# Kernel tuning notes

Measured on AMD Instinct MI355X. Metric: run time of the kernel, lower is better.

The kernel has to match this reference:

```python
import jax, jax.numpy as jnp
import numpy as np

EPS = 1e-5

def conv3x3(x, w, bias=None):
    y = jax.lax.conv_general_dilated(x, w, (1, 1), 'SAME',
                                     dimension_numbers=('NCHW', 'OIHW', 'NCHW'))
    if bias is not None:
        y = y + bias[None, :, None, None]
    return y

def batchnorm(x, g, b):
    m = x.mean((0, 2, 3), keepdims=True)
    v = x.var((0, 2, 3), keepdims=True)
    return (x - m) * jax.lax.rsqrt(v + EPS) * g[None, :, None, None] + b[None, :, None, None]

def deform_sample(x, offset, mask, dg=2):
    # x: [B,C,H,W]; offset: [B,dg*9*2,H,W] (dy,dx interleaved per mmcv); mask: [B,dg*9,H,W]
    B, C, H, W = x.shape
    K = 9
    cg = C // dg
    off = offset.reshape(B, dg, K, 2, H, W)
    dy, dx = off[:, :, :, 0], off[:, :, :, 1]
    m = mask.reshape(B, dg, K, H, W)
    ky = (jnp.repeat(jnp.arange(3), 3) - 1).astype(x.dtype)   # kernel row offset per tap
    kx = (jnp.tile(jnp.arange(3), 3) - 1).astype(x.dtype)     # kernel col offset per tap
    py = dy + jnp.arange(H, dtype=x.dtype)[None, None, None, :, None] + ky[None, None, :, None, None]
    px = dx + jnp.arange(W, dtype=x.dtype)[None, None, None, None, :] + kx[None, None, :, None, None]
    y0 = jnp.floor(py); x0 = jnp.floor(px)
    ly = py - y0; lx = px - x0
    y0i = y0.astype(jnp.int32); x0i = x0.astype(jnp.int32)
    y1i = y0i + 1; x1i = x0i + 1
    def ok(yy, xx):
        return ((yy >= 0) & (yy < H) & (xx >= 0) & (xx < W)).astype(x.dtype)
    xg = x.reshape(B, dg, cg, H * W)
    def gather(yy, xx):
        idx = (jnp.clip(yy, 0, H - 1) * W + jnp.clip(xx, 0, W - 1)).reshape(B, dg, -1)
        g = jax.vmap(jax.vmap(lambda im, ii: im[:, ii]))(xg, idx)   # [B,dg,cg,K*H*W]
        return g.reshape(B, dg, cg, K, H, W)
    w00 = ((1 - ly) * (1 - lx) * ok(y0i, x0i))[:, :, None]
    w01 = ((1 - ly) * lx * ok(y0i, x1i))[:, :, None]
    w10 = (ly * (1 - lx) * ok(y1i, x0i))[:, :, None]
    w11 = (ly * lx * ok(y1i, x1i))[:, :, None]
    val = (gather(y0i, x0i) * w00 + gather(y0i, x1i) * w01 +
           gather(y1i, x0i) * w10 + gather(y1i, x1i) * w11)
    return val * m[:, :, None]   # [B,dg,cg,K,H,W]

def reference(input_v, input_i, off_w, off_b, dconv_w, bn1_g, bn1_b, conv2_w, bn2_g, bn2_b):
    x = jnp.concatenate([input_v, input_i], axis=1)             # [B,C,H,W]
    off_all = conv3x3(x, off_w, off_b)                          # [B,54,H,W]
    o1, o2, mask = jnp.split(off_all, 3, axis=1)
    offset = jnp.concatenate([o1, o2], axis=1)                  # [B,36,H,W]
    mask = jax.nn.sigmoid(mask)                                 # [B,18,H,W]
    sampled = deform_sample(x, offset, mask, dg=2)              # [B,2,cg,9,H,W]
    O = dconv_w.shape[0]
    out = jnp.einsum('bgckhw,ogck->bohw', sampled, dconv_w.reshape(O, 2, -1, 9))
    out = jax.nn.relu(batchnorm(out, bn1_g, bn1_b))
    out = jax.nn.relu(batchnorm(conv3x3(out, conv2_w), bn2_g, bn2_b))
    return out

def setup_inputs() -> dict:
    key = jax.random.key(0)
    ks = jax.random.split(key, 8)
    B, Cm, O, H, W = 4, 128, 128, 64, 64
    C = 2 * Cm
    inp = {}
    inp['input_v'] = jax.random.normal(ks[0], (B, Cm, H, W), jnp.float32)
    inp['input_i'] = jax.random.normal(ks[1], (B, Cm, H, W), jnp.float32)
    # offset/mask conv (zero-init in torch; small random here for a non-trivial reference)
    inp['off_w'] = jax.random.normal(ks[2], (54, C, 3, 3), jnp.float32) * 0.02
    inp['off_b'] = jnp.zeros((54,), jnp.float32)
    inp['dconv_w'] = jax.random.normal(ks[3], (O, C, 3, 3), jnp.float32) * (1.0 / np.sqrt(C * 9))
    inp['bn1_g'] = jnp.ones((O,), jnp.float32)
    inp['bn1_b'] = jnp.zeros((O,), jnp.float32)
    inp['conv2_w'] = jax.random.normal(ks[4], (O, O, 3, 3), jnp.float32) * (1.0 / np.sqrt(O * 9))
    inp['bn2_g'] = jnp.ones((O,), jnp.float32)
    inp['bn2_b'] = jnp.zeros((O,), jnp.float32)
    return inp
```

## Files before the change

### kernel.cpp

```cpp
#include <hip/hip_runtime.h>

#define EPSBN 1e-5f

using s8v = __attribute__((ext_vector_type(8))) short;
using f4v = __attribute__((ext_vector_type(4))) float;

__device__ inline unsigned short f2bf(float f) {
  unsigned u = __float_as_uint(f);
  return (unsigned short)((u + 0x7FFFu + ((u >> 16) & 1u)) >> 16);
}

__global__ __launch_bounds__(256) void k_pack(const float* __restrict__ v, const float* __restrict__ im,
                                              unsigned short* __restrict__ xb) {
  __shared__ float tile[64][33];
  int b = blockIdx.z;
  int hw0 = blockIdx.x * 32;
  int c0 = blockIdx.y * 64;
  int tx = threadIdx.x, ty = threadIdx.y;
#pragma unroll
  for (int i = 0; i < 64; i += 8) {
    int c = c0 + ty + i;
    const float* src = (c < 128) ? (v + ((size_t)b * 128 + c) * 4096)
                                 : (im + ((size_t)b * 128 + (c - 128)) * 4096);
    tile[ty + i][tx] = src[hw0 + tx];
  }
  __syncthreads();
#pragma unroll
  for (int i = 0; i < 32; i += 8) {
    int hw = hw0 + ty + i;
    ushort2 o;
    o.x = f2bf(tile[2 * tx][ty + i]);
    o.y = f2bf(tile[2 * tx + 1][ty + i]);
    *(ushort2*)&xb[((size_t)(b * 4096 + hw)) * 256 + c0 + 2 * tx] = o;
  }
}

__global__ __launch_bounds__(256) void k_wprep_all(const float* __restrict__ w_off,
                                                   const float* __restrict__ w_d,
                                                   const float* __restrict__ w_2,
                                                   unsigned short* __restrict__ wt_off,
                                                   unsigned short* __restrict__ wt_d,
                                                   unsigned short* __restrict__ wt_2) {
  int bid = blockIdx.x, t = threadIdx.x;
  if (bid < 72) {
    int id = bid * 256 + t;
    int lane = id & 63;
    int nb = (id >> 6) & 3;
    int ks = id >> 8;
    int ks2 = ks & 1, tap = (ks >> 1) % 9, cc = ks / 18;
    int o = nb * 16 + (lane & 15);
    int cb = cc * 64 + ks2 * 32 + ((lane >> 4) * 8);
    s8v r;
#pragma unroll
    for (int j = 0; j < 8; ++j) {
      float val = (o < 54) ? w_off[((size_t)o * 256 + cb + j) * 9 + tap] : 0.f;
      r[j] = (short)f2bf(val);
    }
    *(s8v*)&wt_off[(size_t)id * 8] = r;
  } else if (bid < 216) {
    int id = (bid - 72) * 256 + t;
    int lane = id & 63;
    int nb = (id >> 6) & 7;
    int kstep = id >> 9;
    int chunk = kstep >> 2, ks4 = kstep & 3;
    int g = chunk / 9, kk = chunk % 9;
    int o = nb * 16 + (lane & 15);
    int cb = g * 128 + ks4 * 32 + ((lane >> 4) * 8);
    s8v r;
#pragma unroll
    for (int j = 0; j < 8; ++j) r[j] = (short)f2bf(w_d[((size_t)o * 256 + cb + j) * 9 + kk]);
    *(s8v*)&wt_d[(size_t)id * 8] = r;
  } else {
    int id = (bid - 216) * 256 + t;
    int lane = id & 63;
    int nb = (id >> 6) & 7;
    int kstep = id >> 9;
    int ks2 = kstep & 1, tap = (kstep >> 1) % 9, cc = kstep / 18;
    int o = nb * 16 + (lane & 15);
    int cb = cc * 64 + ks2 * 32 + ((lane >> 4) * 8);
    s8v r;
#pragma unroll
    for (int j = 0; j < 8; ++j) r[j] = (short)f2bf(w_2[((size_t)o * 128 + cb + j) * 9 + tap]);
    *(s8v*)&wt_2[(size_t)id * 8] = r;
  }
}

__global__ __launch_bounds__(512, 3) void k_offconv(const unsigned short* __restrict__ xb,
                                                    const unsigned short* __restrict__ wt,
                                                    const float* __restrict__ bias,
                                                    float* __restrict__ off) {
  __shared__ char Xs[102 * 512];
  __shared__ float redx[2048];
  int bid = blockIdx.x;
  int id8 = (bid & 7) * 64 + (bid >> 3);
  int w0 = (id8 & 1) * 32;
  int h = (id8 >> 1) & 63;
  int b = id8 >> 7;
  int t = threadIdx.x;
  int l = t & 63, wv = t >> 6;
  int og = wv & 3, kh = wv >> 2;
  f4v zero = {0.f, 0.f, 0.f, 0.f};
  f4v acc[2] = {zero, zero};

  for (int id = t; id < 3264; id += 512) {
    int tr = id >> 5, oq8 = id & 31;
    int ky = tr / 34, col = tr % 34;
    int hh = h + ky - 1, ww = w0 + col - 1;
    s8v val = {0, 0, 0, 0, 0, 0, 0, 0};
    if ((unsigned)hh < 64u && (unsigned)ww < 64u)
      val = *(const s8v*)&xb[(((size_t)(b * 64 + hh)) * 64 + ww) * 256 + oq8 * 8];
    int byte = (tr * 512 + oq8 * 16) ^ ((tr & 7) << 4);
    *(s8v*)(Xs + byte) = val;
  }
  __syncthreads();
  int khi = l >> 4, lo = l & 15;
#pragma unroll
  for (int tap = 0; tap < 9; ++tap) {
    int ky = tap / 3, kx = tap % 3;
#pragma unroll
    for (int s = 0; s < 4; ++s) {
      int cc = kh * 2 + (s >> 1);
      int ks2 = s & 1;
      int kstep = cc * 18 + tap * 2 + ks2;
      int chb = cc * 128 + ks2 * 64 + khi * 16;
      s8v bfr = *(const s8v*)&wt[((size_t)(kstep * 4 + og) * 64 + l) * 8];
#pragma unroll
      for (int m = 0; m < 2; ++m) {
        int tr = ky * 34 + m * 16 + lo + kx;
        int rbyte = (tr * 512 + chb) ^ ((tr & 7) << 4);
        s8v a = *(const s8v*)(Xs + rbyte);
        acc[m] = __builtin_amdgcn_mfma_f32_16x16x32_bf16(a, bfr, acc[m], 0, 0, 0);
      }
    }
  }
  if (kh == 1) {
#pragma unroll
    for (int m = 0; m < 2; ++m)
#pragma unroll
      for (int j = 0; j < 4; ++j) redx[((og * 64 + l) * 2 + m) * 4 + j] = acc[m][j];
  }
  __syncthreads();
  if (kh == 0) {
    int o = og * 16 + lo;
    int pixb = (b * 64 + h) * 64 + w0;
    if (o < 54) {
      float bi = bias[o];
#pragma unroll
      for (int m = 0; m < 2; ++m)
#pragma unroll
        for (int j = 0; j < 4; ++j) {
          int px = pixb + m * 16 + khi * 4 + j;
          float vv = acc[m][j] + redx[((og * 64 + l) * 2 + m) * 4 + j] + bi;
          if (o >= 36) vv = 1.f / (1.f + __expf(-vv));
          off[(size_t)px * 54 + o] = vv;
        }
    }
  }
}

#define DC_ISSUE(c, V, Q)                                   \
  do {                                                      \
    const unsigned* ip_ = sidx[(c)][px];                    \
    const float* qp_ = swt[(c)][px];                        \
    Q##0 = qp_[0]; Q##1 = qp_[1]; Q##2 = qp_[2]; Q##3 = qp_[3]; \
    V##0 = *(const s8v*)&xb[ip_[0] + chof];                 \
    V##1 = *(const s8v*)&xb[ip_[1] + chof];                 \
    V##2 = *(const s8v*)&xb[ip_[2] + chof];                 \
    V##3 = *(const s8v*)&xb[ip_[3] + chof];                 \
  } while (0)

#define DC_COMMIT(BUF, V, Q)                                            \
  do {                                                                  \
    unsigned rr_[4];                                                    \
    _Pragma("unroll") for (int jp_ = 0; jp_ < 4; ++jp_) {               \
      unsigned w0_ = ((const unsigned*)&V##0)[jp_];                     \
      unsigned w1_ = ((const unsigned*)&V##1)[jp_];                     \
      unsigned w2_ = ((const unsigned*)&V##2)[jp_];                     \
      unsigned w3_ = ((const unsigned*)&V##3)[jp_];                     \
      float e_ = Q##0 * __uint_as_float(w0_ << 16) + Q##1 * __uint_as_float(w1_ << 16) + \
                 Q##2 * __uint_as_float(w2_ << 16) + Q##3 * __uint_as_float(w3_ << 16);  \
      float o_ = Q##0 * __uint_as_float(w0_ & 0xffff0000u) + Q##1 * __uint_as_float(w1_ & 0xffff0000u) + \
                 Q##2 * __uint_as_float(w2_ & 0xffff0000u) + Q##3 * __uint_as_float(w3_ & 0xffff0000u);  \
      unsigned p_;                                                      \
      asm("v_cvt_pk_bf16_f32 %0, %1, %2" : "=v"(p_) : "v"(e_), "v"(o_)); \
      rr_[jp_] = p_;                                                    \
    }                                                                   \
    *(int4*)(&At[BUF][0] + wbyte) = *(int4*)rr_;                        \
  } while (0)

#define LDS_BARRIER()                                        \
  do {                                                       \
    asm volatile("s_waitcnt lgkmcnt(0)" ::: "memory");       \
    __builtin_amdgcn_s_barrier();                            \
  } while (0)

#define DC_MFMA(C, BUF)                                                 \
  do {                                                                  \
    __builtin_amdgcn_s_setprio(1);                                      \
    _Pragma("unroll") for (int ks4_ = 0; ks4_ < 4; ++ks4_) {            \
      int kstep_ = (C) * 4 + ks4_;                                      \
      s8v bfr_ = *(const s8v*)&wt[((size_t)(kstep_ * 8 + og) * 64 + l) * 8]; \
      int chb_ = ks4_ * 64 + khi * 16;                                  \
      _Pragma("unroll") for (int m_ = 0; m_ < 2; ++m_) {                \
        int trA_ = m_ * 16 + lo;                                        \
        int rbyte_ = (trA_ * 256 + chb_) ^ ((trA_ & 7) << 4);           \
        s8v a_ = *(const s8v*)(&At[BUF][0] + rbyte_);                   \
        acc[m_] = __builtin_amdgcn_mfma_f32_16x16x32_bf16(a_, bfr_, acc[m_], 0, 0, 0); \
      }                                                                 \
    }                                                                   \
    __builtin_amdgcn_s_setprio(0);                                      \
  } while (0)

#define DC_PHASE(C, BUF, VI, QI, VC, QC, BUFC)               \
  do {                                                       \
    if ((C) < 15) DC_ISSUE((C) + 3, VI, QI);                 \
    DC_MFMA(C, BUF);                                         \
    if ((C) < 17) DC_COMMIT(BUFC, VC, QC);                   \
    LDS_BARRIER();                                           \
  } while (0)

__global__ __launch_bounds__(512, 4) void k_dconv(const unsigned short* __restrict__ xb,
                                                  const float* __restrict__ off,
                                                  const unsigned short* __restrict__ wt,
                                                  float* __restrict__ y1p,
                                                  float* __restrict__ st1, float* __restrict__ st2) {
  __shared__ unsigned int sidx[18][32][4];
  __shared__ float swt[18][32][4];
  __shared__ char At[3][8192];
  int t = threadIdx.x;
  int l = t & 63, og = t >> 6;
  int bid = blockIdx.x;
  int id8 = (bid & 7) * 64 + (bid >> 3);
  int pixb = id8 * 32;
  int b = pixb >> 12, h = (pixb >> 6) & 63, w0 = pixb & 63;

  for (int id = t; id < 576; id += 512) {
    int chunk = id >> 5, ppx = id & 31;
    int g = chunk / 9, kk = chunk % 9;
    const float* op = off + (size_t)(pixb + ppx) * 54;
    float dy = op[(g * 9 + kk) * 2];
    float dx = op[(g * 9 + kk) * 2 + 1];
    float msk = op[36 + g * 9 + kk];
    float py = dy + (float)(h + kk / 3 - 1);
    float pxf = dx + (float)(w0 + ppx + kk % 3 - 1);
    float y0f = floorf(py), x0f = floorf(pxf);
    float ly = py - y0f, lx = pxf - x0f;
    int y0 = (int)y0f, x0 = (int)x0f;
    int y1 = y0 + 1, x1 = x0 + 1;
    float oky0 = (y0 >= 0 && y0 < 64) ? 1.f : 0.f;
    float oky1 = (y1 >= 0 && y1 < 64) ? 1.f : 0.f;
    float okx0 = (x0 >= 0 && x0 < 64) ? 1.f : 0.f;
    float okx1 = (x1 >= 0 && x1 < 64) ? 1.f : 0.f;
    int y0c = min(max(y0, 0), 63), y1c = min(max(y1, 0), 63);
    int x0c = min(max(x0, 0), 63), x1c = min(max(x1, 0), 63);
    unsigned base = (unsigned)(b * 4096);
    unsigned gofs = (unsigned)(g * 128);
    sidx[chunk][ppx][0] = (base + y0c * 64 + x0c) * 256u + gofs;
    sidx[chunk][ppx][1] = (base + y0c * 64 + x1c) * 256u + gofs;
    sidx[chunk][ppx][2] = (base + y1c * 64 + x0c) * 256u + gofs;
    sidx[chunk][ppx][3] = (base + y1c * 64 + x1c) * 256u + gofs;
    swt[chunk][ppx][0] = (1.f - ly) * (1.f - lx) * oky0 * okx0 * msk;
    swt[chunk][ppx][1] = (1.f - ly) * lx * oky0 * okx1 * msk;
    swt[chunk][ppx][2] = ly * (1.f - lx) * oky1 * okx0 * msk;
    swt[chunk][ppx][3] = ly * lx * oky1 * okx1 * msk;
  }
  __syncthreads();

  int px = t >> 4, oq = t & 15;
  unsigned chof = oq * 8u;
  int wbyte = (px * 256 + oq * 16) ^ ((px & 7) << 4);
  int khi = l >> 4, lo = l & 15;

  s8v va0, va1, va2, va3, vb0, vb1, vb2, vb3, vc0, vc1, vc2, vc3;
  float qa0, qa1, qa2, qa3, qb0, qb1, qb2, qb3, qc0, qc1, qc2, qc3;

  DC_ISSUE(0, va, qa);
  DC_ISSUE(1, vb, qb);
  DC_ISSUE(2, vc, qc);
  DC_COMMIT(0, va, qa);
  LDS_BARRIER();

  f4v zero = {0.f, 0.f, 0.f, 0.f};
  f4v acc[2] = {zero, zero};

  for (int cb = 0; cb < 6; ++cb) {
    int c0 = cb * 3;
    DC_PHASE(c0 + 0, 0, va, qa, vb, qb, 1);
    DC_PHASE(c0 + 1, 1, vb, qb, vc, qc, 2);
    DC_PHASE(c0 + 2, 2, vc, qc, va, qa, 0);
  }

  int o = og * 16 + lo;
  float s1v = 0.f, s2v = 0.f;
#pragma unroll
  for (int m = 0; m < 2; ++m)
#pragma unroll
    for (int j = 0; j < 4; ++j) {
      float vv = acc[m][j];
      y1p[(size_t)(pixb + m * 16 + khi * 4 + j) * 128 + o] = vv;
      s1v += vv; s2v += vv * vv;
    }
  float* red = &swt[0][0][0];
  red[khi * 128 + o] = s1v;
  red[512 + khi * 128 + o] = s2v;
  __syncthreads();
  if (t < 128) {
    float a1 = 0.f, a2 = 0.f;
#pragma unroll
    for (int rr = 0; rr < 4; ++rr) { a1 += red[rr * 128 + t]; a2 += red[512 + rr * 128 + t]; }
    atomicAdd(&st1[t], a1);
    atomicAdd(&st2[t], a2);
  }
}

__global__ __launch_bounds__(256) void k_bnrelu1(const float* __restrict__ yp, const float* __restrict__ s1,
                                                 const float* __restrict__ s2, const float* __restrict__ g,
                                                 const float* __restrict__ bb, unsigned short* __restrict__ yb) {
  __shared__ float sc[128], sh[128];
  int t = threadIdx.x;
  if (t < 128) {
    float m = s1[t] * (1.f / 16384.f);
    float var = s2[t] * (1.f / 16384.f) - m * m;
    float s = g[t] * rsqrtf(var + EPSBN);
    sc[t] = s;
    sh[t] = bb[t] - m * s;
  }
  __syncthreads();
  size_t i = ((size_t)blockIdx.x * 256 + t) * 8;
  int c0 = (int)(i & 127);
  float4 u = *(const float4*)&yp[i];
  float4 v = *(const float4*)&yp[i + 4];
  s8v r;
  r[0] = (short)f2bf(fmaxf(0.f, u.x * sc[c0 + 0] + sh[c0 + 0]));
  r[1] = (short)f2bf(fmaxf(0.f, u.y * sc[c0 + 1] + sh[c0 + 1]));
  r[2] = (short)f2bf(fmaxf(0.f, u.z * sc[c0 + 2] + sh[c0 + 2]));
  r[3] = (short)f2bf(fmaxf(0.f, u.w * sc[c0 + 3] + sh[c0 + 3]));
  r[4] = (short)f2bf(fmaxf(0.f, v.x * sc[c0 + 4] + sh[c0 + 4]));
  r[5] = (short)f2bf(fmaxf(0.f, v.y * sc[c0 + 5] + sh[c0 + 5]));
  r[6] = (short)f2bf(fmaxf(0.f, v.z * sc[c0 + 6] + sh[c0 + 6]));
  r[7] = (short)f2bf(fmaxf(0.f, v.w * sc[c0 + 7] + sh[c0 + 7]));
  *(s8v*)&yb[i] = r;
}

__global__ __launch_bounds__(512, 3) void k_conv2(const unsigned short* __restrict__ yb,
                                                  const unsigned short* __restrict__ wt,
                                                  float* __restrict__ y2p,
                                                  float* __restrict__ st1, float* __restrict__ st2) {
  __shared__ char Bs[102 * 256];
  int bid = blockIdx.x;
  int id8 = (bid & 7) * 64 + (bid >> 3);
  int w0 = (id8 & 1) * 32;
  int h = (id8 >> 1) & 63;
  int b = id8 >> 7;
  int t = threadIdx.x;
  int l = t & 63, og = t >> 6;
  f4v zero = {0.f, 0.f, 0.f, 0.f};
  f4v acc[2] = {zero, zero};

  for (int id = t; id < 1632; id += 512) {
    int tr = id >> 4, oq = id & 15;
    int ky = tr / 34, col = tr % 34;
    int hh = h + ky - 1, ww = w0 + col - 1;
    s8v val = {0, 0, 0, 0, 0, 0, 0, 0};
    if ((unsigned)hh < 64u && (unsigned)ww < 64u)
      val = *(const s8v*)&yb[(((size_t)(b * 64 + hh)) * 64 + ww) * 128 + oq * 8];
    int byte = (tr * 256 + oq * 16) ^ ((tr & 7) << 4);
    *(s8v*)(Bs + byte) = val;
  }
  __syncthreads();
  int khi = l >> 4, lo = l & 15;
#pragma unroll
  for (int tap = 0; tap < 9; ++tap) {
    int ky = tap / 3, kx = tap % 3;
#pragma unroll
    for (int ks4 = 0; ks4 < 4; ++ks4) {
      int kstep = ((ks4 >> 1) * 9 + tap) * 2 + (ks4 & 1);
      s8v bfr = *(const s8v*)&wt[((size_t)(kstep * 8 + og) * 64 + l) * 8];
      int chb = ks4 * 64 + khi * 16;
#pragma unroll
      for (int m = 0; m < 2; ++m) {
        int tr = ky * 34 + m * 16 + lo + kx;
        int rbyte = (tr * 256 + chb) ^ ((tr & 7) << 4);
        s8v a = *(const s8v*)(Bs + rbyte);
        acc[m] = __builtin_amdgcn_mfma_f32_16x16x32_bf16(a, bfr, acc[m], 0, 0, 0);
      }
    }
  }
  __syncthreads();
  int pixb = (b * 64 + h) * 64 + w0;
  int o = og * 16 + lo;
  float s1v = 0.f, s2v = 0.f;
#pragma unroll
  for (int m = 0; m < 2; ++m)
#pragma unroll
    for (int j = 0; j < 4; ++j) {
      float vv = acc[m][j];
      y2p[(size_t)(pixb + m * 16 + khi * 4 + j) * 128 + o] = vv;
      s1v += vv; s2v += vv * vv;
    }
  float* red = (float*)Bs;
  red[khi * 128 + o] = s1v;
  red[512 + khi * 128 + o] = s2v;
  __syncthreads();
  if (t < 128) {
    float a1 = 0.f, a2 = 0.f;
#pragma unroll
    for (int rr = 0; rr < 4; ++rr) { a1 += red[rr * 128 + t]; a2 += red[512 + rr * 128 + t]; }
    atomicAdd(&st1[t], a1);
    atomicAdd(&st2[t], a2);
  }
}

__global__ __launch_bounds__(256) void k_bnrelu2(const float* __restrict__ yp, const float* __restrict__ s1,
                                                 const float* __restrict__ s2, const float* __restrict__ g,
                                                 const float* __restrict__ bb, float* __restrict__ out) {
  __shared__ float sc[128], sh[128];
  __shared__ float buf[64 * 129];
  int t = threadIdx.x;
  if (t < 128) {
    float m = s1[t] * (1.f / 16384.f);
    float var = s2[t] * (1.f / 16384.f) - m * m;
    float s = g[t] * rsqrtf(var + EPSBN);
    sc[t] = s;
    sh[t] = bb[t] - m * s;
  }
  int bh = blockIdx.x;
  int b = bh >> 6, h = bh & 63;
  const float* src = yp + (size_t)bh * 8192;
  for (int i = t; i < 2048; i += 256) {
    float4 v = ((const float4*)src)[i];
    int w = (i * 4) >> 7, o = (i * 4) & 127;
    float* d = &buf[w * 129 + o];
    d[0] = v.x; d[1] = v.y; d[2] = v.z; d[3] = v.w;
  }
  __syncthreads();
  for (int id = t; id < 8192; id += 256) {
    int o = id >> 6, w = id & 63;
    float v = buf[w * 129 + o];
    v = fmaxf(0.f, v * sc[o] + sh[o]);
    out[(((size_t)b * 128 + o) * 64 + h) * 64 + w] = v;
  }
}

extern "C" void kernel_launch(void* const* d_in, const int* in_sizes, int n_in,
                              void* d_out, int out_size, void* d_ws, size_t ws_size,
                              hipStream_t stream) {
  const float* in_v = (const float*)d_in[0];
  const float* in_i = (const float*)d_in[1];
  const float* off_w = (const float*)d_in[2];
  const float* off_b = (const float*)d_in[3];
  const float* dconv_w = (const float*)d_in[4];
  const float* bn1_g = (const float*)d_in[5];
  const float* bn1_b = (const float*)d_in[6];
  const float* conv2_w = (const float*)d_in[7];
  const float* bn2_g = (const float*)d_in[8];
  const float* bn2_b = (const float*)d_in[9];
  float* out = (float*)d_out;

  char* w = (char*)d_ws;
  unsigned short* xb = (unsigned short*)w;      w += (size_t)16384 * 256 * 2;
  float* off_nhwc = (float*)w;                  w += (size_t)16384 * 54 * 4;
  unsigned short* wtf_off = (unsigned short*)w; w += (size_t)18432 * 8 * 2;
  unsigned short* wtf_d = (unsigned short*)w;   w += (size_t)36864 * 8 * 2;
  unsigned short* wtf_2 = (unsigned short*)w;   w += (size_t)18432 * 8 * 2;
  float* y1p = (float*)w;                       w += (size_t)16384 * 128 * 4;
  unsigned short* y1b = (unsigned short*)w;     w += (size_t)16384 * 128 * 2;
  float* y2p = (float*)w;                       w += (size_t)16384 * 128 * 4;
  float* stats = (float*)w;                     w += 512 * 4;

  hipMemsetAsync(stats, 0, 512 * 4, stream);
  k_pack<<<dim3(128, 4, 4), dim3(32, 8), 0, stream>>>(in_v, in_i, xb);
  k_wprep_all<<<288, 256, 0, stream>>>(off_w, dconv_w, conv2_w, wtf_off, wtf_d, wtf_2);
  k_offconv<<<512, 512, 0, stream>>>(xb, wtf_off, off_b, off_nhwc);
  k_dconv<<<512, 512, 0, stream>>>(xb, off_nhwc, wtf_d, y1p, stats, stats + 128);
  k_bnrelu1<<<1024, 256, 0, stream>>>(y1p, stats, stats + 128, bn1_g, bn1_b, y1b);
  k_conv2<<<512, 512, 0, stream>>>(y1b, wtf_2, y2p, stats + 256, stats + 384);
  k_bnrelu2<<<256, 256, 0, stream>>>(y2p, stats + 256, stats + 384, bn2_g, bn2_b, out);
}
```

Measured before the change: 166.2 us.

## Fuse BN1+ReLU into conv2 load, merge prep kernels, store conv2 output as bf16

Merges the input pack, weight prep and stats zeroing into one launch, removing the memset and a separate kernel. BN1 plus ReLU is applied inside conv2 while it loads its halo tile, so the bnrelu1 kernel and its bf16 intermediate are gone. Conv2 now writes bf16 instead of fp32, which halves the traffic into bnrelu2. The trade-offs are that conv2 loads fp32 halos, moving twice the bytes, and recomputes BN for halo pixels. BN2 statistics are also computed from the rounded bf16 values.

```diff
diff --git a/kernel.cpp b/kernel.cpp
--- a/kernel.cpp
+++ b/kernel.cpp
@@ -9,79 +9,88 @@
   unsigned u = __float_as_uint(f);
   return (unsigned short)((u + 0x7FFFu + ((u >> 16) & 1u)) >> 16);
 }
-
-__global__ __launch_bounds__(256) void k_pack(const float* __restrict__ v, const float* __restrict__ im,
-                                              unsigned short* __restrict__ xb) {
-  __shared__ float tile[64][33];
-  int b = blockIdx.z;
-  int hw0 = blockIdx.x * 32;
-  int c0 = blockIdx.y * 64;
-  int tx = threadIdx.x, ty = threadIdx.y;
-#pragma unroll
-  for (int i = 0; i < 64; i += 8) {
-    int c = c0 + ty + i;
-    const float* src = (c < 128) ? (v + ((size_t)b * 128 + c) * 4096)
-                                 : (im + ((size_t)b * 128 + (c - 128)) * 4096);
-    tile[ty + i][tx] = src[hw0 + tx];
-  }
-  __syncthreads();
-#pragma unroll
-  for (int i = 0; i < 32; i += 8) {
-    int hw = hw0 + ty + i;
-    ushort2 o;
-    o.x = f2bf(tile[2 * tx][ty + i]);
-    o.y = f2bf(tile[2 * tx + 1][ty + i]);
-    *(ushort2*)&xb[((size_t)(b * 4096 + hw)) * 256 + c0 + 2 * tx] = o;
-  }
-}
-
-__global__ __launch_bounds__(256) void k_wprep_all(const float* __restrict__ w_off,
-                                                   const float* __restrict__ w_d,
-                                                   const float* __restrict__ w_2,
-                                                   unsigned short* __restrict__ wt_off,
-                                                   unsigned short* __restrict__ wt_d,
-                                                   unsigned short* __restrict__ wt_2) {
+__device__ inline float bf2f(unsigned short h) {
+  return __uint_as_float(((unsigned)h) << 16);
+}
+
+__global__ __launch_bounds__(256) void k_prep(const float* __restrict__ v, const float* __restrict__ im,
+                                              const float* __restrict__ w_off, const float* __restrict__ w_d,
+                                              const float* __restrict__ w_2,
+                                              unsigned short* __restrict__ xb,
+                                              unsigned short* __restrict__ wt_off,
+                                              unsigned short* __restrict__ wt_d,
+                                              unsigned short* __restrict__ wt_2,
+                                              float* __restrict__ stats) {
   int bid = blockIdx.x, t = threadIdx.x;
-  if (bid < 72) {
-    int id = bid * 256 + t;
-    int lane = id & 63;
-    int nb = (id >> 6) & 3;
-    int ks = id >> 8;
-    int ks2 = ks & 1, tap = (ks >> 1) % 9, cc = ks / 18;
-    int o = nb * 16 + (lane & 15);
-    int cb = cc * 64 + ks2 * 32 + ((lane >> 4) * 8);
-    s8v r;
-#pragma unroll
-    for (int j = 0; j < 8; ++j) {
-      float val = (o < 54) ? w_off[((size_t)o * 256 + cb + j) * 9 + tap] : 0.f;
-      r[j] = (short)f2bf(val);
-    }
-    *(s8v*)&wt_off[(size_t)id * 8] = r;
-  } else if (bid < 216) {
-    int id = (bid - 72) * 256 + t;
-    int lane = id & 63;
-    int nb = (id >> 6) & 7;
-    int kstep = id >> 9;
-    int chunk = kstep >> 2, ks4 = kstep & 3;
-    int g = chunk / 9, kk = chunk % 9;
-    int o = nb * 16 + (lane & 15);
-    int cb = g * 128 + ks4 * 32 + ((lane >> 4) * 8);
-    s8v r;
-#pragma unroll
-    for (int j = 0; j < 8; ++j) r[j] = (short)f2bf(w_d[((size_t)o * 256 + cb + j) * 9 + kk]);
-    *(s8v*)&wt_d[(size_t)id * 8] = r;
+  if (bid < 2048) {
+    __shared__ float tile[64][33];
+    int b = bid >> 9;
+    int rem = bid & 511;
+    int c0 = (rem >> 7) * 64;
+    int hw0 = (rem & 127) * 32;
+    int tx = t & 31, ty = t >> 5;
+#pragma unroll
+    for (int i = 0; i < 64; i += 8) {
+      int c = c0 + ty + i;
+      const float* src = (c < 128) ? (v + ((size_t)b * 128 + c) * 4096)
+                                   : (im + ((size_t)b * 128 + (c - 128)) * 4096);
+      tile[ty + i][tx] = src[hw0 + tx];
+    }
+    __syncthreads();
+#pragma unroll
+    for (int i = 0; i < 32; i += 8) {
+      int hw = hw0 + ty + i;
+      ushort2 o;
+      o.x = f2bf(tile[2 * tx][ty + i]);
+      o.y = f2bf(tile[2 * tx + 1][ty + i]);
+      *(ushort2*)&xb[((size_t)(b * 4096 + hw)) * 256 + c0 + 2 * tx] = o;
+    }
+  } else if (bid < 2336) {
+    int wb = bid - 2048;
+    if (wb < 72) {
+      int id = wb * 256 + t;
+      int lane = id & 63;
+      int nb = (id >> 6) & 3;
+      int ks = id >> 8;
+      int ks2 = ks & 1, tap = (ks >> 1) % 9, cc = ks / 18;
+      int o = nb * 16 + (lane & 15);
+      int cb = cc * 64 + ks2 * 32 + ((lane >> 4) * 8);
+      s8v r;
+#pragma unroll
+      for (int j = 0; j < 8; ++j) {
+        float val = (o < 54) ? w_off[((size_t)o * 256 + cb + j) * 9 + tap] : 0.f;
+        r[j] = (short)f2bf(val);
+      }
+      *(s8v*)&wt_off[(size_t)id * 8] = r;
+    } else if (wb < 216) {
+      int id = (wb - 72) * 256 + t;
+      int lane = id & 63;
+      int nb = (id >> 6) & 7;
+      int kstep = id >> 9;
+      int chunk = kstep >> 2, ks4 = kstep & 3;
+      int g = chunk / 9, kk = chunk % 9;
+      int o = nb * 16 + (lane & 15);
+      int cb = g * 128 + ks4 * 32 + ((lane >> 4) * 8);
+      s8v r;
+#pragma unroll
+      for (int j = 0; j < 8; ++j) r[j] = (short)f2bf(w_d[((size_t)o * 256 + cb + j) * 9 + kk]);
+      *(s8v*)&wt_d[(size_t)id * 8] = r;
+    } else {
+      int id = (wb - 216) * 256 + t;
+      int lane = id & 63;
+      int nb = (id >> 6) & 7;
+      int kstep = id >> 9;
+      int ks2 = kstep & 1, tap = (kstep >> 1) % 9, cc = kstep / 18;
+      int o = nb * 16 + (lane & 15);
+      int cb = cc * 64 + ks2 * 32 + ((lane >> 4) * 8);
+      s8v r;
+#pragma unroll
+      for (int j = 0; j < 8; ++j) r[j] = (short)f2bf(w_2[((size_t)o * 128 + cb + j) * 9 + tap]);
+      *(s8v*)&wt_2[(size_t)id * 8] = r;
+    }
   } else {
-    int id = (bid - 216) * 256 + t;
-    int lane = id & 63;
-    int nb = (id >> 6) & 7;
-    int kstep = id >> 9;
-    int ks2 = kstep & 1, tap = (kstep >> 1) % 9, cc = kstep / 18;
-    int o = nb * 16 + (lane & 15);
-    int cb = cc * 64 + ks2 * 32 + ((lane >> 4) * 8);
-    s8v r;
-#pragma unroll
-    for (int j = 0; j < 8; ++j) r[j] = (short)f2bf(w_2[((size_t)o * 128 + cb + j) * 9 + tap]);
-    *(s8v*)&wt_2[(size_t)id * 8] = r;
+    stats[t] = 0.f;
+    stats[256 + t] = 0.f;
   }
 }
 
@@ -313,40 +322,14 @@
   }
 }
 
-__global__ __launch_bounds__(256) void k_bnrelu1(const float* __restrict__ yp, const float* __restrict__ s1,
-                                                 const float* __restrict__ s2, const float* __restrict__ g,
-                                                 const float* __restrict__ bb, unsigned short* __restrict__ yb) {
-  __shared__ float sc[128], sh[128];
-  int t = threadIdx.x;
-  if (t < 128) {
-    float m = s1[t] * (1.f / 16384.f);
-    float var = s2[t] * (1.f / 16384.f) - m * m;
-    float s = g[t] * rsqrtf(var + EPSBN);
-    sc[t] = s;
-    sh[t] = bb[t] - m * s;
-  }
-  __syncthreads();
-  size_t i = ((size_t)blockIdx.x * 256 + t) * 8;
-  int c0 = (int)(i & 127);
-  float4 u = *(const float4*)&yp[i];
-  float4 v = *(const float4*)&yp[i + 4];
-  s8v r;
-  r[0] = (short)f2bf(fmaxf(0.f, u.x * sc[c0 + 0] + sh[c0 + 0]));
-  r[1] = (short)f2bf(fmaxf(0.f, u.y * sc[c0 + 1] + sh[c0 + 1]));
-  r[2] = (short)f2bf(fmaxf(0.f, u.z * sc[c0 + 2] + sh[c0 + 2]));
-  r[3] = (short)f2bf(fmaxf(0.f, u.w * sc[c0 + 3] + sh[c0 + 3]));
-  r[4] = (short)f2bf(fmaxf(0.f, v.x * sc[c0 + 4] + sh[c0 + 4]));
-  r[5] = (short)f2bf(fmaxf(0.f, v.y * sc[c0 + 5] + sh[c0 + 5]));
-  r[6] = (short)f2bf(fmaxf(0.f, v.z * sc[c0 + 6] + sh[c0 + 6]));
-  r[7] = (short)f2bf(fmaxf(0.f, v.w * sc[c0 + 7] + sh[c0 + 7]));
-  *(s8v*)&yb[i] = r;
-}
-
-__global__ __launch_bounds__(512, 3) void k_conv2(const unsigned short* __restrict__ yb,
+__global__ __launch_bounds__(512, 3) void k_conv2(const float* __restrict__ y1p,
                                                   const unsigned short* __restrict__ wt,
-                                                  float* __restrict__ y2p,
+                                                  const float* __restrict__ s1, const float* __restrict__ s2,
+                                                  const float* __restrict__ g1, const float* __restrict__ b1,
+                                                  unsigned short* __restrict__ y2b,
                                                   float* __restrict__ st1, float* __restrict__ st2) {
   __shared__ char Bs[102 * 256];
+  __shared__ float sc[128], sh[128];
   int bid = blockIdx.x;
   int id8 = (bid & 7) * 64 + (bid >> 3);
   int w0 = (id8 & 1) * 32;
@@ -354,6 +337,14 @@
   int b = id8 >> 7;
   int t = threadIdx.x;
   int l = t & 63, og = t >> 6;
+  if (t < 128) {
+    float m = s1[t] * (1.f / 16384.f);
+    float var = s2[t] * (1.f / 16384.f) - m * m;
+    float s = g1[t] * rsqrtf(var + EPSBN);
+    sc[t] = s;
+    sh[t] = b1[t] - m * s;
+  }
+  __syncthreads();
   f4v zero = {0.f, 0.f, 0.f, 0.f};
   f4v acc[2] = {zero, zero};
 
@@ -362,8 +353,20 @@
     int ky = tr / 34, col = tr % 34;
     int hh = h + ky - 1, ww = w0 + col - 1;
     s8v val = {0, 0, 0, 0, 0, 0, 0, 0};
-    if ((unsigned)hh < 64u && (unsigned)ww < 64u)
-      val = *(const s8v*)&yb[(((size_t)(b * 64 + hh)) * 64 + ww) * 128 + oq * 8];
+    if ((unsigned)hh < 64u && (unsigned)ww < 64u) {
+      const float* src = y1p + (((size_t)(b * 64 + hh)) * 64 + ww) * 128 + oq * 8;
+      float4 u = *(const float4*)src;
+      float4 w4 = *(const float4*)(src + 4);
+      int c = oq * 8;
+      val[0] = (short)f2bf(fmaxf(0.f, u.x * sc[c + 0] + sh[c + 0]));
+      val[1] = (short)f2bf(fmaxf(0.f, u.y * sc[c + 1] + sh[c + 1]));
+      val[2] = (short)f2bf(fmaxf(0.f, u.z * sc[c + 2] + sh[c + 2]));
+      val[3] = (short)f2bf(fmaxf(0.f, u.w * sc[c + 3] + sh[c + 3]));
+      val[4] = (short)f2bf(fmaxf(0.f, w4.x * sc[c + 4] + sh[c + 4]));
+      val[5] = (short)f2bf(fmaxf(0.f, w4.y * sc[c + 5] + sh[c + 5]));
+      val[6] = (short)f2bf(fmaxf(0.f, w4.z * sc[c + 6] + sh[c + 6]));
+      val[7] = (short)f2bf(fmaxf(0.f, w4.w * sc[c + 7] + sh[c + 7]));
+    }
     int byte = (tr * 256 + oq * 16) ^ ((tr & 7) << 4);
     *(s8v*)(Bs + byte) = val;
   }
@@ -394,9 +397,10 @@
   for (int m = 0; m < 2; ++m)
 #pragma unroll
     for (int j = 0; j < 4; ++j) {
-      float vv = acc[m][j];
-      y2p[(size_t)(pixb + m * 16 + khi * 4 + j) * 128 + o] = vv;
-      s1v += vv; s2v += vv * vv;
+      unsigned short us = f2bf(acc[m][j]);
+      y2b[(size_t)(pixb + m * 16 + khi * 4 + j) * 128 + o] = us;
+      float vr = bf2f(us);
+      s1v += vr; s2v += vr * vr;
     }
   float* red = (float*)Bs;
   red[khi * 128 + o] = s1v;
@@ -411,9 +415,10 @@
   }
 }
 
-__global__ __launch_bounds__(256) void k_bnrelu2(const float* __restrict__ yp, const float* __restrict__ s1,
-                                                 const float* __restrict__ s2, const float* __restrict__ g,
-                                                 const float* __restrict__ bb, float* __restrict__ out) {
+__global__ __launch_bounds__(256) void k_bnrelu2(const unsigned short* __restrict__ yb,
+                                                 const float* __restrict__ s1, const float* __restrict__ s2,
+                                                 const float* __restrict__ g, const float* __restrict__ bb,
+                                                 float* __restrict__ out) {
   __shared__ float sc[128], sh[128];
   __shared__ float buf[64 * 129];
   int t = threadIdx.x;
@@ -426,12 +431,14 @@
   }
   int bh = blockIdx.x;
   int b = bh >> 6, h = bh & 63;
-  const float* src = yp + (size_t)bh * 8192;
-  for (int i = t; i < 2048; i += 256) {
-    float4 v = ((const float4*)src)[i];
-    int w = (i * 4) >> 7, o = (i * 4) & 127;
+  const unsigned short* src = yb + (size_t)bh * 8192;
+  for (int i = t; i < 1024; i += 256) {
+    s8v v = *(const s8v*)&src[i * 8];
+    int w = i >> 4;
+    int o = (i & 15) * 8;
     float* d = &buf[w * 129 + o];
-    d[0] = v.x; d[1] = v.y; d[2] = v.z; d[3] = v.w;
+#pragma unroll
+    for (int j = 0; j < 8; ++j) d[j] = bf2f((unsigned short)v[j]);
   }
   __syncthreads();
   for (int id = t; id < 8192; id += 256) {
@@ -464,16 +471,12 @@
   unsigned short* wtf_d = (unsigned short*)w;   w += (size_t)36864 * 8 * 2;
   unsigned short* wtf_2 = (unsigned short*)w;   w += (size_t)18432 * 8 * 2;
   float* y1p = (float*)w;                       w += (size_t)16384 * 128 * 4;
-  unsigned short* y1b = (unsigned short*)w;     w += (size_t)16384 * 128 * 2;
-  float* y2p = (float*)w;                       w += (size_t)16384 * 128 * 4;
+  unsigned short* y2b = (unsigned short*)w;     w += (size_t)16384 * 128 * 2;
   float* stats = (float*)w;                     w += 512 * 4;
 
-  hipMemsetAsync(stats, 0, 512 * 4, stream);
-  k_pack<<<dim3(128, 4, 4), dim3(32, 8), 0, stream>>>(in_v, in_i, xb);
-  k_wprep_all<<<288, 256, 0, stream>>>(off_w, dconv_w, conv2_w, wtf_off, wtf_d, wtf_2);
+  k_prep<<<2337, 256, 0, stream>>>(in_v, in_i, off_w, dconv_w, conv2_w, xb, wtf_off, wtf_d, wtf_2, stats);
   k_offconv<<<512, 512, 0, stream>>>(xb, wtf_off, off_b, off_nhwc);
   k_dconv<<<512, 512, 0, stream>>>(xb, off_nhwc, wtf_d, y1p, stats, stats + 128);
-  k_bnrelu1<<<1024, 256, 0, stream>>>(y1p, stats, stats + 128, bn1_g, bn1_b, y1b);
-  k_conv2<<<512, 512, 0, stream>>>(y1b, wtf_2, y2p, stats + 256, stats + 384);
-  k_bnrelu2<<<256, 256, 0, stream>>>(y2p, stats + 256, stats + 384, bn2_g, bn2_b, out);
-}
+  k_conv2<<<512, 512, 0, stream>>>(y1p, wtf_2, stats, stats + 128, bn1_g, bn1_b, y2b, stats + 256, stats + 384);
+  k_bnrelu2<<<256, 256, 0, stream>>>(y2b, stats + 256, stats + 384, bn2_g, bn2_b, out);
+}
```

Result: faster. 162.4 us (-2.3%).
